# Performance work log

Measured on AMD Instinct MI355X. Metric: run time of the kernel, lower is better.

Reference implementation:

```python
import jax, jax.numpy as jnp
import numpy as np

B, F, G, L, C = 32768, 512, 16, 64, 1000  # batch, feature_dim, n_groups, labels/group, num_classes


def setup_inputs() -> dict:
    key = jax.random.key(0)
    k1, k2, k3, k4, k5 = jax.random.split(key, 5)
    features = jax.random.normal(k1, (B, F), dtype=jnp.float32)
    group_probs = jax.random.uniform(k2, (B, G), dtype=jnp.float32)
    # stacked per-group Linear heads: W[g] is the (L, F) weight of head g, b[g] its bias
    W = jax.random.normal(k3, (G, L, F), dtype=jnp.float32) / np.sqrt(F).astype(np.float32)
    b = jax.random.normal(k4, (G, L), dtype=jnp.float32) * 0.01
    # group_to_labels: label_ids[g, j] = shared class id that head g's j-th output maps to
    label_ids = jax.random.randint(k5, (G, L), 0, C, dtype=jnp.int32)
    return {"features": features, "group_probs": group_probs, "W": W, "b": b,
            "label_ids": label_ids}


def reference(features, group_probs, W, b, label_ids):
    # all per-group linear heads as one batched GEMM: [B,G,L]
    group_logits = jnp.einsum('bf,glf->bgl', features, W) + b
    # weight each group's logits by its group probability
    weighted = group_probs[:, :, None] * group_logits          # [B, G, L]
    # scatter-add into the shared logit tensor (duplicate class ids accumulate)
    flat_idx = label_ids.reshape(-1)                            # [G*L]
    logits = jnp.zeros((features.shape[0], C), dtype=features.dtype)
    logits = logits.at[:, flat_idx].add(weighted.reshape(features.shape[0], -1))
    return logits
```

## Files before the change

### kernel.cpp

```cpp
#include <hip/hip_runtime.h>
#include <stdint.h>

#define B_SZ   32768
#define F_SZ   512
#define G_SZ   16
#define L_SZ   64
#define N_COLS 1024
#define C_SZ   1000
#define M_TILE 32
#define A_STRIDE 520
#define SMEM_BYTES 65536

typedef __attribute__((ext_vector_type(8))) short short8;
typedef __attribute__((ext_vector_type(4))) float floatx4;

__device__ __forceinline__ unsigned short f2bf(float f) {
    unsigned int x = __float_as_uint(f);
    x += 0x7fffu + ((x >> 16) & 1u);
    return (unsigned short)(x >> 16);
}

__global__ __launch_bounds__(1024) void build_csr_kernel(const int* __restrict__ label_ids,
                                                         const float* __restrict__ bias,
                                                         int* __restrict__ off,
                                                         int* __restrict__ list,
                                                         float* __restrict__ bias_p,
                                                         unsigned char* __restrict__ g_perm) {
    __shared__ int cnt[1024];
    __shared__ int cur[1024];
    const int t = threadIdx.x;
    cnt[t] = 0;
    __syncthreads();
    const int lbl = label_ids[t];
    atomicAdd(&cnt[lbl], 1);
    __syncthreads();
    int v = cnt[t];
    #pragma unroll
    for (int d = 1; d < 1024; d <<= 1) {
        int u = (t >= d) ? cnt[t - d] : 0;
        __syncthreads();
        v += u;
        cnt[t] = v;
        __syncthreads();
    }
    int ex = (t == 0) ? 0 : cnt[t - 1];
    cur[t] = ex;
    if (t <= C_SZ) off[t] = (t == 0) ? 0 : cnt[t - 1];
    __syncthreads();
    int pos = atomicAdd(&cur[lbl], 1);
    list[pos]   = t;
    bias_p[pos] = bias[t];
    g_perm[pos] = (unsigned char)(t >> 6);
}

__global__ __launch_bounds__(256) void convert_w_kernel(const float* __restrict__ W,
                                                        const int* __restrict__ list,
                                                        unsigned short* __restrict__ Wb) {
    int idx = blockIdx.x * 256 + threadIdx.x;
    int row = idx >> 7;
    int c4  = idx & 127;
    int src = list[row];
    const float4* W4 = (const float4*)W;
    float4 v = W4[src * 128 + c4];
    ushort4 u = make_ushort4(f2bf(v.x), f2bf(v.y), f2bf(v.z), f2bf(v.w));
    ((ushort4*)Wb)[idx] = u;
}

__global__ __launch_bounds__(1024, 8) void mhc_main_kernel(
        const float* __restrict__ feat,
        const float* __restrict__ gp,
        const unsigned short* __restrict__ Wb,
        const float* __restrict__ bias_p,
        const int* __restrict__ off,
        const unsigned char* __restrict__ g_perm,
        float* __restrict__ out)
{
    __shared__ __align__(16) char smem[SMEM_BYTES];
    __shared__ float gp_s[M_TILE * G_SZ];
    __shared__ float bias_s[N_COLS];
    __shared__ unsigned char g_s[N_COLS];

    unsigned short* As = (unsigned short*)smem;
    float* WT = (float*)smem;

    const int t    = threadIdx.x;
    const int wave = t >> 6;
    const int lane = t & 63;
    const int m16  = lane & 15;
    const int quad = lane >> 4;
    const int r0   = blockIdx.x * M_TILE;

    if (t < M_TILE * G_SZ) gp_s[t] = gp[r0 * G_SZ + t];
    bias_s[t] = bias_p[t];
    g_s[t]    = g_perm[t];

    {
        const floatx4* f4 = (const floatx4*)(feat + (size_t)r0 * F_SZ);
        #pragma unroll
        for (int i = 0; i < 4; ++i) {
            int idx = t + i * 1024;
            int row = idx >> 7;
            int c4  = idx & 127;
            floatx4 v = __builtin_nontemporal_load(f4 + idx);
            ushort4 u = make_ushort4(f2bf(v[0]), f2bf(v[1]), f2bf(v[2]), f2bf(v[3]));
            *(ushort4*)(As + row * A_STRIDE + c4 * 4) = u;
        }
    }
    __syncthreads();

    const floatx4 zero = {0.f, 0.f, 0.f, 0.f};
    floatx4 acc[2][4];
    #pragma unroll
    for (int i = 0; i < 2; ++i)
        #pragma unroll
        for (int j = 0; j < 4; ++j) acc[i][j] = zero;

    const unsigned short* aBase = As + m16 * A_STRIDE + quad * 8;
    const unsigned short* bBase = Wb + (size_t)(wave * 64 + m16) * F_SZ + quad * 8;

    #pragma unroll 2
    for (int kt = 0; kt < 16; ++kt) {
        short8 a0 = *(const short8*)(aBase + kt * 32);
        short8 a1 = *(const short8*)(aBase + 16 * A_STRIDE + kt * 32);
        #pragma unroll
        for (int ct = 0; ct < 4; ++ct) {
            short8 b = *(const short8*)(bBase + ct * 16 * F_SZ + kt * 32);
            acc[0][ct] = __builtin_amdgcn_mfma_f32_16x16x32_bf16(a0, b, acc[0][ct], 0, 0, 0);
            acc[1][ct] = __builtin_amdgcn_mfma_f32_16x16x32_bf16(a1, b, acc[1][ct], 0, 0, 0);
        }
    }

    int e0 = 0, e1 = 0;
    if (t < C_SZ) { e0 = off[t]; e1 = off[t + 1]; }

    #pragma unroll
    for (int p = 0; p < 2; ++p) {
        __syncthreads();
        #pragma unroll
        for (int ct = 0; ct < 4; ++ct) {
            int col = wave * 64 + ct * 16 + m16;
            int g   = g_s[col];
            float bi = bias_s[col];
            int slot = quad ^ ((col ^ (col >> 2)) & 3);
            floatx4 w;
            #pragma unroll
            for (int r = 0; r < 4; ++r) {
                int rl = quad * 4 + r;
                w[r] = gp_s[(p * 16 + rl) * G_SZ + g] * (acc[p][ct][r] + bi);
            }
            *(floatx4*)(WT + col * 16 + slot * 4) = w;
        }
        __syncthreads();
        if (t < C_SZ) {
            float s[16];
            #pragma unroll
            for (int i = 0; i < 16; ++i) s[i] = 0.f;
            for (int j = e0; j < e1; ++j) {
                int sw = (j ^ (j >> 2)) & 3;
                const float* cbase = WT + j * 16;
                #pragma unroll
                for (int q = 0; q < 4; ++q) {
                    floatx4 v = *(const floatx4*)(cbase + ((q ^ sw) << 2));
                    s[q * 4 + 0] += v[0];
                    s[q * 4 + 1] += v[1];
                    s[q * 4 + 2] += v[2];
                    s[q * 4 + 3] += v[3];
                }
            }
            size_t rowg = (size_t)(r0 + p * 16);
            #pragma unroll
            for (int rr = 0; rr < 16; ++rr)
                __builtin_nontemporal_store(s[rr], out + (rowg + rr) * C_SZ + t);
        }
    }
}

extern "C" void kernel_launch(void* const* d_in, const int* in_sizes, int n_in,
                              void* d_out, int out_size, void* d_ws, size_t ws_size,
                              hipStream_t stream) {
    const float* feat  = (const float*)d_in[0];
    const float* gp    = (const float*)d_in[1];
    const float* W     = (const float*)d_in[2];
    const float* bias  = (const float*)d_in[3];
    const int* labels  = (const int*)d_in[4];
    float* out = (float*)d_out;

    unsigned short* Wb = (unsigned short*)d_ws;
    char* base = (char*)d_ws + (1 << 20);
    int* off             = (int*)base;
    int* list            = (int*)(base + 4096);
    float* bias_p        = (float*)(base + 8192);
    unsigned char* g_prm = (unsigned char*)(base + 12288);

    build_csr_kernel<<<1, 1024, 0, stream>>>(labels, bias, off, list, bias_p, g_prm);
    convert_w_kernel<<<(N_COLS * F_SZ / 4) / 256, 256, 0, stream>>>(W, list, Wb);
    mhc_main_kernel<<<B_SZ / M_TILE, 1024, 0, stream>>>(feat, gp, Wb, bias_p, off, g_prm, out);
}
```

Before: 304.7 us.

## Process two row tiles per block with register prefetch of next tile

Each block now handles two consecutive 32-row tiles and prefetches the next tile's features and group probs into registers while the current tile's epilogue runs, overlapping global loads with scatter/store work. Barriers are replaced by a custom sched_barrier + lgkmcnt wait + s_barrier sequence that does not wait on outstanding vector memory loads, so the prefetch can stay in flight. Output stores switch from nontemporal to regular stores. The block count halves, which reduces parallelism (512 blocks of 1024 threads) and raises register pressure from holding prefetch registers across the epilogue.

```diff
diff --git a/kernel.cpp b/kernel.cpp
--- a/kernel.cpp
+++ b/kernel.cpp
@@ -8,6 +8,7 @@
 #define N_COLS 1024
 #define C_SZ   1000
 #define M_TILE 32
+#define TILES_PER_BLK 2
 #define A_STRIDE 520
 #define SMEM_BYTES 65536
 
@@ -18,6 +19,13 @@
     unsigned int x = __float_as_uint(f);
     x += 0x7fffu + ((x >> 16) & 1u);
     return (unsigned short)(x >> 16);
+}
+
+__device__ __forceinline__ void barrier_lgkm() {
+    __builtin_amdgcn_sched_barrier(0);
+    asm volatile("s_waitcnt lgkmcnt(0)" ::: "memory");
+    __builtin_amdgcn_s_barrier();
+    __builtin_amdgcn_sched_barrier(0);
 }
 
 __global__ __launch_bounds__(1024) void build_csr_kernel(const int* __restrict__ label_ids,
@@ -88,89 +96,118 @@
     const int lane = t & 63;
     const int m16  = lane & 15;
     const int quad = lane >> 4;
-    const int r0   = blockIdx.x * M_TILE;
-
-    if (t < M_TILE * G_SZ) gp_s[t] = gp[r0 * G_SZ + t];
+
     bias_s[t] = bias_p[t];
     g_s[t]    = g_perm[t];
-
-    {
-        const floatx4* f4 = (const floatx4*)(feat + (size_t)r0 * F_SZ);
-        #pragma unroll
-        for (int i = 0; i < 4; ++i) {
-            int idx = t + i * 1024;
-            int row = idx >> 7;
-            int c4  = idx & 127;
-            floatx4 v = __builtin_nontemporal_load(f4 + idx);
-            ushort4 u = make_ushort4(f2bf(v[0]), f2bf(v[1]), f2bf(v[2]), f2bf(v[3]));
-            *(ushort4*)(As + row * A_STRIDE + c4 * 4) = u;
-        }
-    }
-    __syncthreads();
-
-    const floatx4 zero = {0.f, 0.f, 0.f, 0.f};
-    floatx4 acc[2][4];
-    #pragma unroll
-    for (int i = 0; i < 2; ++i)
-        #pragma unroll
-        for (int j = 0; j < 4; ++j) acc[i][j] = zero;
-
-    const unsigned short* aBase = As + m16 * A_STRIDE + quad * 8;
-    const unsigned short* bBase = Wb + (size_t)(wave * 64 + m16) * F_SZ + quad * 8;
-
-    #pragma unroll 2
-    for (int kt = 0; kt < 16; ++kt) {
-        short8 a0 = *(const short8*)(aBase + kt * 32);
-        short8 a1 = *(const short8*)(aBase + 16 * A_STRIDE + kt * 32);
-        #pragma unroll
-        for (int ct = 0; ct < 4; ++ct) {
-            short8 b = *(const short8*)(bBase + ct * 16 * F_SZ + kt * 32);
-            acc[0][ct] = __builtin_amdgcn_mfma_f32_16x16x32_bf16(a0, b, acc[0][ct], 0, 0, 0);
-            acc[1][ct] = __builtin_amdgcn_mfma_f32_16x16x32_bf16(a1, b, acc[1][ct], 0, 0, 0);
-        }
-    }
-
     int e0 = 0, e1 = 0;
     if (t < C_SZ) { e0 = off[t]; e1 = off[t + 1]; }
 
+    const floatx4* f4 = (const floatx4*)feat;
+    floatx4 pf0, pf1, pf2, pf3;
+    float pgp = 0.f;
+    {
+        size_t base = (size_t)blockIdx.x * TILES_PER_BLK * M_TILE * (F_SZ / 4);
+        pf0 = __builtin_nontemporal_load(f4 + base + t);
+        pf1 = __builtin_nontemporal_load(f4 + base + t + 1024);
+        pf2 = __builtin_nontemporal_load(f4 + base + t + 2048);
+        pf3 = __builtin_nontemporal_load(f4 + base + t + 3072);
+        if (t < M_TILE * G_SZ)
+            pgp = gp[(size_t)blockIdx.x * TILES_PER_BLK * M_TILE * G_SZ + t];
+    }
+
     #pragma unroll
-    for (int p = 0; p < 2; ++p) {
-        __syncthreads();
+    for (int it = 0; it < TILES_PER_BLK; ++it) {
+        const int tile = blockIdx.x * TILES_PER_BLK + it;
+        const int r0   = tile * M_TILE;
+
+        barrier_lgkm();
+
+        {
+            floatx4 pr[4] = {pf0, pf1, pf2, pf3};
+            #pragma unroll
+            for (int i = 0; i < 4; ++i) {
+                int idx = t + i * 1024;
+                int row = idx >> 7;
+                int c4  = idx & 127;
+                ushort4 u = make_ushort4(f2bf(pr[i][0]), f2bf(pr[i][1]),
+                                         f2bf(pr[i][2]), f2bf(pr[i][3]));
+                *(ushort4*)(As + row * A_STRIDE + c4 * 4) = u;
+            }
+            if (t < M_TILE * G_SZ) gp_s[t] = pgp;
+        }
+        barrier_lgkm();
+
+        const floatx4 zero = {0.f, 0.f, 0.f, 0.f};
+        floatx4 acc[2][4];
         #pragma unroll
-        for (int ct = 0; ct < 4; ++ct) {
-            int col = wave * 64 + ct * 16 + m16;
-            int g   = g_s[col];
-            float bi = bias_s[col];
-            int slot = quad ^ ((col ^ (col >> 2)) & 3);
-            floatx4 w;
-            #pragma unroll
-            for (int r = 0; r < 4; ++r) {
-                int rl = quad * 4 + r;
-                w[r] = gp_s[(p * 16 + rl) * G_SZ + g] * (acc[p][ct][r] + bi);
-            }
-            *(floatx4*)(WT + col * 16 + slot * 4) = w;
-        }
-        __syncthreads();
-        if (t < C_SZ) {
-            float s[16];
-            #pragma unroll
-            for (int i = 0; i < 16; ++i) s[i] = 0.f;
-            for (int j = e0; j < e1; ++j) {
-                int sw = (j ^ (j >> 2)) & 3;
-                const float* cbase = WT + j * 16;
+        for (int i = 0; i < 2; ++i)
+            #pragma unroll
+            for (int j = 0; j < 4; ++j) acc[i][j] = zero;
+
+        const unsigned short* aBase = As + m16 * A_STRIDE + quad * 8;
+        const unsigned short* bBase = Wb + (size_t)(wave * 64 + m16) * F_SZ + quad * 8;
+
+        #pragma unroll 2
+        for (int kt = 0; kt < 16; ++kt) {
+            short8 a0 = *(const short8*)(aBase + kt * 32);
+            short8 a1 = *(const short8*)(aBase + 16 * A_STRIDE + kt * 32);
+            #pragma unroll
+            for (int ct = 0; ct < 4; ++ct) {
+                short8 b = *(const short8*)(bBase + ct * 16 * F_SZ + kt * 32);
+                acc[0][ct] = __builtin_amdgcn_mfma_f32_16x16x32_bf16(a0, b, acc[0][ct], 0, 0, 0);
+                acc[1][ct] = __builtin_amdgcn_mfma_f32_16x16x32_bf16(a1, b, acc[1][ct], 0, 0, 0);
+            }
+        }
+
+        if (it + 1 < TILES_PER_BLK) {
+            size_t base = (size_t)(tile + 1) * M_TILE * (F_SZ / 4);
+            pf0 = __builtin_nontemporal_load(f4 + base + t);
+            pf1 = __builtin_nontemporal_load(f4 + base + t + 1024);
+            pf2 = __builtin_nontemporal_load(f4 + base + t + 2048);
+            pf3 = __builtin_nontemporal_load(f4 + base + t + 3072);
+            if (t < M_TILE * G_SZ)
+                pgp = gp[(size_t)(tile + 1) * M_TILE * G_SZ + t];
+        }
+
+        #pragma unroll
+        for (int p = 0; p < 2; ++p) {
+            barrier_lgkm();
+            #pragma unroll
+            for (int ct = 0; ct < 4; ++ct) {
+                int col = wave * 64 + ct * 16 + m16;
+                int g   = g_s[col];
+                float bi = bias_s[col];
+                int slot = quad ^ ((col ^ (col >> 2)) & 3);
+                floatx4 w;
                 #pragma unroll
-                for (int q = 0; q < 4; ++q) {
-                    floatx4 v = *(const floatx4*)(cbase + ((q ^ sw) << 2));
-                    s[q * 4 + 0] += v[0];
-                    s[q * 4 + 1] += v[1];
-                    s[q * 4 + 2] += v[2];
-                    s[q * 4 + 3] += v[3];
+                for (int r = 0; r < 4; ++r) {
+                    int rl = quad * 4 + r;
+                    w[r] = gp_s[(p * 16 + rl) * G_SZ + g] * (acc[p][ct][r] + bi);
                 }
-            }
-            size_t rowg = (size_t)(r0 + p * 16);
-            #pragma unroll
-            for (int rr = 0; rr < 16; ++rr)
-                __builtin_nontemporal_store(s[rr], out + (rowg + rr) * C_SZ + t);
+                *(floatx4*)(WT + col * 16 + slot * 4) = w;
+            }
+            barrier_lgkm();
+            if (t < C_SZ) {
+                float s[16];
+                #pragma unroll
+                for (int i = 0; i < 16; ++i) s[i] = 0.f;
+                for (int j = e0; j < e1; ++j) {
+                    int sw = (j ^ (j >> 2)) & 3;
+                    const float* cbase = WT + j * 16;
+                    #pragma unroll
+                    for (int q = 0; q < 4; ++q) {
+                        floatx4 v = *(const floatx4*)(cbase + ((q ^ sw) << 2));
+                        s[q * 4 + 0] += v[0];
+                        s[q * 4 + 1] += v[1];
+                        s[q * 4 + 2] += v[2];
+                        s[q * 4 + 3] += v[3];
+                    }
+                }
+                size_t rowg = (size_t)(r0 + p * 16);
+                #pragma unroll
+                for (int rr = 0; rr < 16; ++rr)
+                    out[(rowg + rr) * C_SZ + t] = s[rr];
+            }
         }
     }
 }
@@ -194,5 +231,5 @@
 
     build_csr_kernel<<<1, 1024, 0, stream>>>(labels, bias, off, list, bias_p, g_prm);
     convert_w_kernel<<<(N_COLS * F_SZ / 4) / 256, 256, 0, stream>>>(W, list, Wb);
-    mhc_main_kernel<<<B_SZ / M_TILE, 1024, 0, stream>>>(feat, gp, Wb, bias_p, off, g_prm, out);
-}
+    mhc_main_kernel<<<B_SZ / (M_TILE * TILES_PER_BLK), 1024, 0, stream>>>(feat, gp, Wb, bias_p, off, g_prm, out);
+}
```

Measured after the change: 333.0 us. 9.3% more time.
